# Optimization experiments

Hardware: AMD Instinct MI355X
Metric: run time of the kernel (lower is better)

Reference implementation:

```python
import jax, jax.numpy as jnp
import numpy as np

H_DIM = 1024
N_HEADS = 16
HEAD_D = H_DIM // N_HEADS  # 64


def setup_inputs() -> dict:
    key = jax.random.key(0)
    ks = jax.random.split(key, 10)
    B, T, C = 2, 2048, H_DIM
    init = 1.0 / np.sqrt(C)  # lecun_normal-scale stand-in
    src = jax.random.normal(ks[0], (B, T, C), dtype=jnp.float32)
    mask = jnp.ones((B, T), dtype=jnp.float32)  # unused when causal
    Wq = jax.random.normal(ks[1], (C, H_DIM), dtype=jnp.float32) * init
    Wk = jax.random.normal(ks[2], (C, H_DIM), dtype=jnp.float32) * init
    Wv = jax.random.normal(ks[3], (C, H_DIM), dtype=jnp.float32) * init
    Wo = jax.random.normal(ks[4], (H_DIM, H_DIM), dtype=jnp.float32) * init
    bq = jnp.zeros((H_DIM,), jnp.float32)
    bk = jnp.zeros((H_DIM,), jnp.float32)
    bv = jnp.zeros((H_DIM,), jnp.float32)
    bo = jnp.zeros((H_DIM,), jnp.float32)
    return {"src": src, "mask": mask, "Wq": Wq, "bq": bq, "Wk": Wk, "bk": bk,
            "Wv": Wv, "bv": bv, "Wo": Wo, "bo": bo}


def reference(src, mask, Wq, bq, Wk, bk, Wv, bv, Wo, bo):
    # MaskedCausalAttention forward, deterministic=True (dropout = identity),
    # use_causal_mask=True.
    B, T, C = src.shape
    N, D = N_HEADS, HEAD_D
    # q,k,v: [B, N, T, D]
    q = (src @ Wq + bq).reshape(B, T, N, D).transpose(0, 2, 1, 3)
    k = (src @ Wk + bk).reshape(B, T, N, D).transpose(0, 2, 1, 3)
    v = (src @ Wv + bv).reshape(B, T, N, D).transpose(0, 2, 1, 3)
    # scores: [B, N, T, T]
    scores = jnp.einsum('bntd,bnsd->bnts', q, k) / jnp.sqrt(jnp.float32(D))
    causal = jnp.tril(jnp.ones((T, T), dtype=bool))[None, None]
    scores = jnp.where(causal, scores, -jnp.inf)
    probs = jax.nn.softmax(scores, axis=-1)
    attn = jnp.einsum('bnts,bnsd->bntd', probs, v)  # [B, N, T, D]
    attn = attn.transpose(0, 2, 1, 3).reshape(B, T, N * D)
    return attn @ Wo + bo
```

## Files before the change

kernel.cpp:

```cpp
#include <hip/hip_runtime.h>
#include <hip/hip_bf16.h>

typedef __hip_bfloat16 bf16;
typedef __attribute__((ext_vector_type(8))) short short8;
typedef __attribute__((ext_vector_type(4))) float f32x4;

#define BATCH 2
#define SEQ   2048
#define HDIM  1024
#define NHEAD 16
#define DHEAD 64
#define MROWS (BATCH*SEQ)

#define QSCALE 0.18033688f
#define EXP2F(x) __builtin_amdgcn_exp2f(x)

static __device__ __forceinline__ short f2bs(float x) {
    __hip_bfloat16 h = (__hip_bfloat16)x;
    return *reinterpret_cast<short*>(&h);
}
static __device__ __forceinline__ unsigned int pk2(float a, float b) {
    __hip_bfloat162 h = __float22bfloat162_rn(make_float2(a, b));
    return *reinterpret_cast<unsigned int*>(&h);
}

static __device__ __forceinline__ void gload16(const void* g, void* l) {
    __builtin_amdgcn_global_load_lds(
        (const __attribute__((address_space(1))) unsigned int*)g,
        (__attribute__((address_space(3))) unsigned int*)l, 16, 0, 0);
}

__global__ __launch_bounds__(256) void prep1(const float* __restrict__ src,
        const float* __restrict__ Wq, const float* __restrict__ Wk,
        const float* __restrict__ Wv, const float* __restrict__ Wo,
        short* __restrict__ Sb, short* __restrict__ WT,
        short* __restrict__ WoT)
{
    __shared__ float t[64][65];
    const int bx = blockIdx.x, tid = threadIdx.x;
    if (bx < 4096) {
        int i = bx * 256 + tid;
        float4 v = ((const float4*)src)[i];
        ushort4 o;
        o.x = (unsigned short)f2bs(v.x);
        o.y = (unsigned short)f2bs(v.y);
        o.z = (unsigned short)f2bs(v.z);
        o.w = (unsigned short)f2bs(v.w);
        ((ushort4*)Sb)[i] = o;
        return;
    }
    const int tb = bx - 4096;
    const int wsel = tb >> 8;
    const float* W = (wsel == 0) ? Wq : (wsel == 1) ? Wk : (wsel == 2) ? Wv : Wo;
    short* dst = (wsel < 3) ? WT : WoT;
    const int roff = (wsel < 3) ? wsel * 1024 : 0;
    const int t8 = tb & 255;
    const int n0 = (t8 & 15) * 64, k0 = (t8 >> 4) * 64;
#pragma unroll
    for (int i = 0; i < 16; i++) {
        int idx = tid + i * 256, r = idx >> 6, c = idx & 63;
        t[r][c] = W[(size_t)(k0 + r) * HDIM + n0 + c];
    }
    __syncthreads();
#pragma unroll
    for (int i = 0; i < 16; i++) {
        int idx = tid + i * 256, c = idx >> 6, r = idx & 63;
        dst[(size_t)(roff + n0 + c) * HDIM + k0 + r] = f2bs(t[r][c]);
    }
}

__global__ __launch_bounds__(512, 2) void gemm_qkv(const short* __restrict__ A,
        const short* __restrict__ Bt,
        const float* __restrict__ bq, const float* __restrict__ bk,
        const float* __restrict__ bv,
        short* __restrict__ Qout, short* __restrict__ Kout,
        short* __restrict__ Vtout)
{
    __shared__ short SM[2][28672];
    const int tid = threadIdx.x, lane = tid & 63, w = tid >> 6;
    const int quad = lane >> 4, l15 = lane & 15;
    const int m0 = blockIdx.y * 256, n0 = blockIdx.x * 192;
    const int wr = w >> 1, wc = w & 1;

    static const unsigned char CTAB[8][7] = {
        { 0,  1,  2,  3, 32 + 0,  32 + 1,  32 + 6 },
        { 4,  5,  6,  7, 32 + 2,  32 + 3,  32 + 7 },
        { 8,  9, 10, 11, 32 + 4,  32 + 5,  32 + 8 },
        {12, 13, 14, 15, 32 + 12, 32 + 13, 32 + 9 },
        {16, 17, 18, 19, 32 + 14, 32 + 10, 32 + 11},
        {20, 21, 22, 23, 32 + 15, 32 + 18, 32 + 19},
        {24, 25, 26, 27, 32 + 16, 32 + 20, 32 + 21},
        {28, 29, 30, 31, 32 + 17, 32 + 22, 32 + 23}
    };

    const short* gp[7];
    int lo[7];
#pragma unroll
    for (int i = 0; i < 7; i++) {
        int c = CTAB[w][i];
        if (c < 32) {
            gp[i] = A + (size_t)(m0 + (c >> 1) * 16 + l15) * HDIM
                      + (c & 1) * 32 + quad * 8;
            lo[i] = c * 512;
        } else {
            int v = c - 32;
            gp[i] = Bt + (size_t)(n0 + (v >> 1) * 16 + l15) * HDIM
                       + (v & 1) * 32 + quad * 8;
            lo[i] = 16384 + v * 512;
        }
    }

    f32x4 acc[4][6];
#pragma unroll
    for (int i = 0; i < 4; i++)
#pragma unroll
        for (int j = 0; j < 6; j++) acc[i][j] = (f32x4){0.f, 0.f, 0.f, 0.f};

#pragma unroll
    for (int i = 0; i < 7; i++) { gload16(gp[i], &SM[0][lo[i]]); gp[i] += 64; }

    short8 af[4][2];
    for (int t = 0; t < 16; ++t) {
        const short* Tb = SM[t & 1];
        short* Sn = SM[(t + 1) & 1];

        asm volatile("s_waitcnt vmcnt(1)" ::: "memory");
        __builtin_amdgcn_s_barrier();

#pragma unroll
        for (int mi = 0; mi < 4; mi++)
#pragma unroll
            for (int kh = 0; kh < 2; kh++)
                af[mi][kh] = *(const short8*)
                    &Tb[((wr * 4 + mi) * 2 + kh) * 512 + lane * 8];
        short8 bf01[3][2];
#pragma unroll
        for (int nn = 0; nn < 3; nn++)
#pragma unroll
            for (int kh = 0; kh < 2; kh++)
                bf01[nn][kh] = *(const short8*)
                    &Tb[16384 + ((wc * 6 + nn) * 2 + kh) * 512 + lane * 8];

        if (t < 15) {
#pragma unroll
            for (int i = 0; i < 7; i++) { gload16(gp[i], Sn + lo[i]); gp[i] += 64; }
        }

        __builtin_amdgcn_s_setprio(1);
#pragma unroll
        for (int nn = 0; nn < 3; nn++)
#pragma unroll
            for (int mi = 0; mi < 4; mi++)
#pragma unroll
                for (int kh = 0; kh < 2; kh++)
                    acc[mi][nn] = __builtin_amdgcn_mfma_f32_16x16x32_bf16(
                        af[mi][kh], bf01[nn][kh], acc[mi][nn], 0, 0, 0);
        __builtin_amdgcn_s_setprio(0);

        if (t < 15) asm volatile("s_waitcnt vmcnt(7)" ::: "memory");
        else        asm volatile("s_waitcnt vmcnt(0)" ::: "memory");

        short8 bf23[3][2];
#pragma unroll
        for (int nn = 0; nn < 3; nn++)
#pragma unroll
            for (int kh = 0; kh < 2; kh++)
                bf23[nn][kh] = *(const short8*)
                    &Tb[16384 + ((wc * 6 + 3 + nn) * 2 + kh) * 512 + lane * 8];

        __builtin_amdgcn_s_setprio(1);
#pragma unroll
        for (int nn = 0; nn < 3; nn++)
#pragma unroll
            for (int mi = 0; mi < 4; mi++)
#pragma unroll
                for (int kh = 0; kh < 2; kh++)
                    acc[mi][3 + nn] = __builtin_amdgcn_mfma_f32_16x16x32_bf16(
                        af[mi][kh], bf23[nn][kh], acc[mi][3 + nn], 0, 0, 0);
        __builtin_amdgcn_s_setprio(0);
    }

#pragma unroll
    for (int mi = 0; mi < 4; mi++) {
        int mB = m0 + wr * 64 + mi * 16 + quad * 4;
        int bb = mB >> 11, tt = mB & 2047;
#pragma unroll
        for (int ni = 0; ni < 6; ni++) {
            int n = n0 + wc * 96 + ni * 16 + l15;
            int rg = n >> 10, nl = n & 1023;
            if (rg == 0) {
                float bbv = bq[nl];
#pragma unroll
                for (int r = 0; r < 4; r++)
                    Qout[(size_t)(mB + r) * HDIM + nl] =
                        f2bs((acc[mi][ni][r] + bbv) * QSCALE);
            } else if (rg == 1) {
                float bbv = bk[nl];
#pragma unroll
                for (int r = 0; r < 4; r++)
                    Kout[(size_t)(mB + r) * HDIM + nl] =
                        f2bs(acc[mi][ni][r] + bbv);
            } else {
                float bvv = bv[nl];
                int h = nl >> 6, d = nl & 63;
                size_t base = ((size_t)((bb * NHEAD + h) * DHEAD + d)) * SEQ + tt;
                ushort4 pk;
                pk.x = (unsigned short)f2bs(acc[mi][ni][0] + bvv);
                pk.y = (unsigned short)f2bs(acc[mi][ni][1] + bvv);
                pk.z = (unsigned short)f2bs(acc[mi][ni][2] + bvv);
                pk.w = (unsigned short)f2bs(acc[mi][ni][3] + bvv);
                *(ushort4*)(Vtout + base) = pk;
            }
        }
    }
}

__global__ __launch_bounds__(512) void attn_mfma(const short* __restrict__ Qb,
        const short* __restrict__ Kb, const short* __restrict__ Vt,
        short* __restrict__ Ab,
        float* __restrict__ Opart, float* __restrict__ Psum)
{
    __shared__ short SMEM[25600];
    const int tid = threadIdx.x, lane = tid & 63, w = tid >> 6;
    const int quad = lane >> 4, l15 = lane & 15;
    const int L = blockIdx.x;

    static const signed char S_TAB[24] =
        {15,15, 7,14,14,13,13, 6,12,12,11,11, 5,10,10, 9, 9, 4, 8, 8, 3, 2, 1, 0};
    static const signed char H_TAB[24] =
        { 0, 1,-1, 0, 1, 0, 1,-1, 0, 1, 0, 1,-1, 0, 1, 0, 1,-1, 0, 1,-1,-1,-1,-1};

    const int pair = (L & 7) + 8 * ((L >> 3) & 3);
    const int u = L >> 5;
    const int b = pair >> 4, head = pair & 15;
    const int sblk = S_TAB[u];
    const int half = H_TAB[u];
    const int it0   = (half == 1) ? (sblk + 1) : 0;
    const int itEnd = (half == 0) ? (sblk + 1) : (2 * sblk + 2);
    const int nj = itEnd - it0;

    const short* Kbh = Kb + (size_t)b * SEQ * HDIM + head * DHEAD;
    const short* Vth = Vt + (size_t)(b * NHEAD + head) * DHEAD * SEQ;
    short* Pw = SMEM + 16384 + w * 1152;

    const int s_w = 2 * sblk + (w >> 2);
    const int rho = w * 16 + l15;
    const int qr = sblk * 128 + rho;

    const short* qptr = Qb + (size_t)(b * SEQ + qr) * HDIM + head * DHEAD + quad * 8;
    short8 bq0 = *(const short8*)qptr;
    short8 bq1 = *(const short8*)(qptr + 32);

    const short* gp[2];
    int stp[2], ldo[2];
#pragma unroll
    for (int i = 0; i < 2; i++) {
        int c8 = w * 2 + i;
        if (c8 < 8) {
            int t = c8 >> 1, h = c8 & 1;
            gp[i] = Kbh + (size_t)(t * 16 + l15) * HDIM + h * 32 + quad * 8;
            stp[i] = 64 * HDIM;
        } else {
            int c = c8 - 8, dt = c >> 1, kh = c & 1;
            gp[i] = Vth + (size_t)(dt * 16 + l15) * SEQ + kh * 32 + quad * 8;
            stp[i] = 64;
        }
        ldo[i] = c8 * 512;
        gp[i] += (size_t)it0 * stp[i];
    }

    f32x4 o[4];
#pragma unroll
    for (int dt = 0; dt < 4; dt++) o[dt] = (f32x4){0.f, 0.f, 0.f, 0.f};
    float psum = 0.f;

#pragma unroll
    for (int i = 0; i < 2; i++) { gload16(gp[i], &SMEM[ldo[i]]); gp[i] += stp[i]; }

    for (int j = 0; j < nj; ++j) {
        const int cur = j & 1;
        short* Ks = &SMEM[cur * 8192];
        short* Vs = Ks + 4096;

        if (j + 1 < nj) {
            short* nb = &SMEM[(cur ^ 1) * 8192];
#pragma unroll
            for (int i = 0; i < 2; i++) { gload16(gp[i], nb + ldo[i]); gp[i] += stp[i]; }
            asm volatile("s_waitcnt vmcnt(2)" ::: "memory");
        } else {
            asm volatile("s_waitcnt vmcnt(0)" ::: "memory");
        }
        __builtin_amdgcn_s_barrier();

        const int itg = it0 + j;
        const int s0 = itg * 64;
        f32x4 sv[4];
        __builtin_amdgcn_s_setprio(1);
#pragma unroll
        for (int t = 0; t < 4; t++) {
            sv[t] = (f32x4){0.f, 0.f, 0.f, 0.f};
            short8 k0 = *(const short8*)&Ks[(t * 2) * 512 + lane * 8];
            short8 k1 = *(const short8*)&Ks[(t * 2 + 1) * 512 + lane * 8];
            sv[t] = __builtin_amdgcn_mfma_f32_16x16x32_bf16(k0, bq0, sv[t], 0, 0, 0);
            sv[t] = __builtin_amdgcn_mfma_f32_16x16x32_bf16(k1, bq1, sv[t], 0, 0, 0);
        }
        __builtin_amdgcn_s_setprio(0);

        float p[16];
        if (itg >= s_w) {
#pragma unroll
            for (int t = 0; t < 4; t++)
#pragma unroll
                for (int r = 0; r < 4; r++) {
                    int key = s0 + t * 16 + quad * 4 + r;
                    p[t * 4 + r] = (key <= qr) ? EXP2F(sv[t][r]) : 0.f;
                }
        } else {
#pragma unroll
            for (int t = 0; t < 4; t++)
#pragma unroll
                for (int r = 0; r < 4; r++)
                    p[t * 4 + r] = EXP2F(sv[t][r]);
        }
#pragma unroll
        for (int i = 0; i < 16; i++) psum += p[i];

#pragma unroll
        for (int t = 0; t < 4; t++) {
            uint2 u2;
            u2.x = pk2(p[t * 4],     p[t * 4 + 1]);
            u2.y = pk2(p[t * 4 + 2], p[t * 4 + 3]);
            *(uint2*)&Pw[l15 * 72 + t * 16 + quad * 4] = u2;
        }
        short8 bp0 = *(const short8*)&Pw[l15 * 72 + quad * 8];
        short8 bp1 = *(const short8*)&Pw[l15 * 72 + 32 + quad * 8];

        __builtin_amdgcn_s_setprio(1);
#pragma unroll
        for (int dt = 0; dt < 4; dt++) {
            short8 av0 = *(const short8*)&Vs[(dt * 2) * 512 + lane * 8];
            short8 av1 = *(const short8*)&Vs[(dt * 2 + 1) * 512 + lane * 8];
            o[dt] = __builtin_amdgcn_mfma_f32_16x16x32_bf16(av0, bp0, o[dt], 0, 0, 0);
            o[dt] = __builtin_amdgcn_mfma_f32_16x16x32_bf16(av1, bp1, o[dt], 0, 0, 0);
        }
        __builtin_amdgcn_s_setprio(0);
        __builtin_amdgcn_s_barrier();
    }

    float lrow = psum + __shfl_xor(psum, 16);
    lrow += __shfl_xor(lrow, 32);

    if (half >= 0) {
        const int tile = (pair * 8 + (sblk - 8)) * 2 + half;
        float* Ot = Opart + (size_t)tile * 8192;
#pragma unroll
        for (int dt = 0; dt < 4; dt++)
            *(f32x4*)&Ot[rho * 64 + dt * 16 + quad * 4] = o[dt];
        if (quad == 0) Psum[(pair * 8 + (sblk - 8)) * 256 + half * 128 + rho] = lrow;
        return;
    }

    const float inv = 1.f / lrow;
    const size_t obase = (size_t)(b * SEQ + qr) * HDIM + head * DHEAD;
#pragma unroll
    for (int dt = 0; dt < 4; dt++) {
        uint2 u2;
        u2.x = pk2(o[dt][0] * inv, o[dt][1] * inv);
        u2.y = pk2(o[dt][2] * inv, o[dt][3] * inv);
        *(uint2*)&Ab[obase + dt * 16 + quad * 4] = u2;
    }
}

__global__ __launch_bounds__(256) void combine(const float* __restrict__ Opart,
        const float* __restrict__ Psum, short* __restrict__ Ab)
{
    const int bxx = blockIdx.x;
    const int pair = bxx & 31, si = bxx >> 5;
    const int b = pair >> 4, head = pair & 15;
    const int tid = threadIdx.x;
    const int row = tid >> 1, dq = (tid & 1) * 32;

    const size_t t0 = ((size_t)(pair * 8 + si) * 2) * 8192;
    const float* O0 = Opart + t0;
    const float* O1 = O0 + 8192;
    const int p0 = (pair * 8 + si) * 256;
    const float inv = 1.f / (Psum[p0 + row] + Psum[p0 + 128 + row]);

    const int qrow = (8 + si) * 128 + row;
    const size_t obase = (size_t)(b * SEQ + qrow) * HDIM + head * DHEAD + dq;
#pragma unroll
    for (int g = 0; g < 8; g++) {
        float4 a = *(const float4*)&O0[row * 64 + dq + g * 4];
        float4 c = *(const float4*)&O1[row * 64 + dq + g * 4];
        ushort4 pk;
        pk.x = (unsigned short)f2bs((a.x + c.x) * inv);
        pk.y = (unsigned short)f2bs((a.y + c.y) * inv);
        pk.z = (unsigned short)f2bs((a.z + c.z) * inv);
        pk.w = (unsigned short)f2bs((a.w + c.w) * inv);
        *(ushort4*)&Ab[obase + g * 4] = pk;
    }
}

__global__ __launch_bounds__(512) void gemm_o(const short* __restrict__ A,
        const short* __restrict__ Bt, const float* __restrict__ bo,
        float* __restrict__ Out)
{
    __shared__ short SM[2 * 16384];
    const int tid = threadIdx.x, lane = tid & 63, w = tid >> 6;
    const int quad = lane >> 4, l15 = lane & 15;
    const int m0 = blockIdx.y * 128, n0 = blockIdx.x * 128;
    const int wr = w >> 2, wc = w & 3;

    const short* gsrc[4];
    short* ldst[4];
#pragma unroll
    for (int i = 0; i < 4; i++) {
        int c8 = w * 4 + i;
        if (c8 < 16) {
            gsrc[i] = A + (size_t)(m0 + (c8 >> 1) * 16 + l15) * HDIM
                        + (c8 & 1) * 32 + quad * 8;
            ldst[i] = &SM[c8 * 512];
        } else {
            int v = c8 - 16;
            gsrc[i] = Bt + (size_t)(n0 + (v >> 1) * 16 + l15) * HDIM
                         + (v & 1) * 32 + quad * 8;
            ldst[i] = &SM[8192 + v * 512];
        }
    }

    f32x4 acc[4][2];
#pragma unroll
    for (int i = 0; i < 4; i++)
#pragma unroll
        for (int j = 0; j < 2; j++) acc[i][j] = (f32x4){0.f, 0.f, 0.f, 0.f};

#pragma unroll
    for (int i = 0; i < 4; i++) { gload16(gsrc[i], ldst[i]); gsrc[i] += 64; }

    for (int kk = 0; kk < 16; ++kk) {
        const int cur = kk & 1;
        if (kk < 15) {
            const int nb = (cur ^ 1) * 16384;
#pragma unroll
            for (int i = 0; i < 4; i++) { gload16(gsrc[i], ldst[i] + nb); gsrc[i] += 64; }
            asm volatile("s_waitcnt vmcnt(4)" ::: "memory");
        } else {
            asm volatile("s_waitcnt vmcnt(0)" ::: "memory");
        }
        __builtin_amdgcn_s_barrier();

        const short* Asb = &SM[cur * 16384];
        const short* Bsb = Asb + 8192;
#pragma unroll
        for (int kh = 0; kh < 2; kh++) {
            short8 af[4], bfr[2];
#pragma unroll
            for (int mi = 0; mi < 4; mi++)
                af[mi] = *(const short8*)&Asb[((wr * 4 + mi) * 2 + kh) * 512 + lane * 8];
#pragma unroll
            for (int ni = 0; ni < 2; ni++)
                bfr[ni] = *(const short8*)&Bsb[((wc * 2 + ni) * 2 + kh) * 512 + lane * 8];
#pragma unroll
            for (int mi = 0; mi < 4; mi++)
#pragma unroll
                for (int ni = 0; ni < 2; ni++)
                    acc[mi][ni] = __builtin_amdgcn_mfma_f32_16x16x32_bf16(
                                      af[mi], bfr[ni], acc[mi][ni], 0, 0, 0);
        }
        __builtin_amdgcn_s_barrier();
    }

#pragma unroll
    for (int mi = 0; mi < 4; mi++) {
        int mB = m0 + (wr * 4 + mi) * 16 + quad * 4;
#pragma unroll
        for (int ni = 0; ni < 2; ni++) {
            int n = n0 + (wc * 2 + ni) * 16 + l15;
            float bb = bo[n];
#pragma unroll
            for (int r = 0; r < 4; r++)
                Out[(size_t)(mB + r) * HDIM + n] = acc[mi][ni][r] + bb;
        }
    }
}

extern "C" void kernel_launch(void* const* d_in, const int* in_sizes, int n_in,
                              void* d_out, int out_size, void* d_ws, size_t ws_size,
                              hipStream_t stream)
{
    const float* src = (const float*)d_in[0];
    const float* Wq = (const float*)d_in[2];
    const float* bq = (const float*)d_in[3];
    const float* Wk = (const float*)d_in[4];
    const float* bk = (const float*)d_in[5];
    const float* Wv = (const float*)d_in[6];
    const float* bv = (const float*)d_in[7];
    const float* Wo = (const float*)d_in[8];
    const float* bo = (const float*)d_in[9];
    float* out = (float*)d_out;

    short* Sb   = (short*)d_ws;
    short* Qb   = Sb + (size_t)MROWS * HDIM;
    short* Kb   = Qb + (size_t)MROWS * HDIM;
    short* Vt   = Kb + (size_t)MROWS * HDIM;
    short* WoT  = Vt + (size_t)MROWS * HDIM;
    short* WT   = (short*)d_out;
    short* Ab   = Qb;
    float* Opart = (float*)d_out;
    float* Psum  = (float*)Sb;

    prep1<<<dim3(4096 + 1024), dim3(256), 0, stream>>>(src, Wq, Wk, Wv, Wo, Sb, WT, WoT);

    gemm_qkv<<<dim3(16, 16), dim3(512), 0, stream>>>(Sb, WT, bq, bk, bv, Qb, Kb, Vt);

    attn_mfma<<<dim3(768), dim3(512), 0, stream>>>(Qb, Kb, Vt, Ab, Opart, Psum);

    combine<<<dim3(256), dim3(256), 0, stream>>>(Opart, Psum, Ab);

    gemm_o<<<dim3(8, 32), dim3(512), 0, stream>>>(Ab, WoT, bo, out);
}
```

Before: 192.6 us.

## Double attention query tile to 256 rows with 1024-thread blocks

Each attention block now covers 256 query rows with 16 waves instead of 128 rows with 8 waves. This halves the grid and lets each K/V tile loaded into shared memory be reused by twice as many query rows, with one load per wave per iteration. The schedule tables, split-half ranges, partial-output layout and combine kernel are rescaled to match. In exchange there are fewer blocks to balance across CUs, the work per block is coarser, and the larger LDS footprint and 1024-thread blocks may lower occupancy.

```diff
diff --git a/kernel.cpp b/kernel.cpp
--- a/kernel.cpp
+++ b/kernel.cpp
@@ -215,58 +215,55 @@
     }
 }
 
-__global__ __launch_bounds__(512) void attn_mfma(const short* __restrict__ Qb,
+__global__ __launch_bounds__(1024) void attn_mfma(const short* __restrict__ Qb,
         const short* __restrict__ Kb, const short* __restrict__ Vt,
         short* __restrict__ Ab,
         float* __restrict__ Opart, float* __restrict__ Psum)
 {
-    __shared__ short SMEM[25600];
+    __shared__ short SMEM[34816];
     const int tid = threadIdx.x, lane = tid & 63, w = tid >> 6;
     const int quad = lane >> 4, l15 = lane & 15;
     const int L = blockIdx.x;
 
-    static const signed char S_TAB[24] =
-        {15,15, 7,14,14,13,13, 6,12,12,11,11, 5,10,10, 9, 9, 4, 8, 8, 3, 2, 1, 0};
-    static const signed char H_TAB[24] =
-        { 0, 1,-1, 0, 1, 0, 1,-1, 0, 1, 0, 1,-1, 0, 1, 0, 1,-1, 0, 1,-1,-1,-1,-1};
+    static const signed char S_TAB[12] = {7,7,3,6,6,5,5,2,4,4,1,0};
+    static const signed char H_TAB[12] = {0,1,-1,0,1,0,1,-1,0,1,-1,-1};
 
     const int pair = (L & 7) + 8 * ((L >> 3) & 3);
     const int u = L >> 5;
     const int b = pair >> 4, head = pair & 15;
     const int sblk = S_TAB[u];
     const int half = H_TAB[u];
-    const int it0   = (half == 1) ? (sblk + 1) : 0;
-    const int itEnd = (half == 0) ? (sblk + 1) : (2 * sblk + 2);
+    const int it0   = (half == 1) ? (2 * sblk + 2) : 0;
+    const int itEnd = (half == 0) ? (2 * sblk + 2) : (4 * sblk + 4);
     const int nj = itEnd - it0;
 
     const short* Kbh = Kb + (size_t)b * SEQ * HDIM + head * DHEAD;
     const short* Vth = Vt + (size_t)(b * NHEAD + head) * DHEAD * SEQ;
     short* Pw = SMEM + 16384 + w * 1152;
 
-    const int s_w = 2 * sblk + (w >> 2);
+    const int s_w = 4 * sblk + (w >> 2);
     const int rho = w * 16 + l15;
-    const int qr = sblk * 128 + rho;
+    const int qr = sblk * 256 + rho;
 
     const short* qptr = Qb + (size_t)(b * SEQ + qr) * HDIM + head * DHEAD + quad * 8;
     short8 bq0 = *(const short8*)qptr;
     short8 bq1 = *(const short8*)(qptr + 32);
 
-    const short* gp[2];
-    int stp[2], ldo[2];
-#pragma unroll
-    for (int i = 0; i < 2; i++) {
-        int c8 = w * 2 + i;
+    const short* gp0;
+    int stp0, ldo0;
+    {
+        int c8 = w;
         if (c8 < 8) {
             int t = c8 >> 1, h = c8 & 1;
-            gp[i] = Kbh + (size_t)(t * 16 + l15) * HDIM + h * 32 + quad * 8;
-            stp[i] = 64 * HDIM;
+            gp0 = Kbh + (size_t)(t * 16 + l15) * HDIM + h * 32 + quad * 8;
+            stp0 = 64 * HDIM;
         } else {
             int c = c8 - 8, dt = c >> 1, kh = c & 1;
-            gp[i] = Vth + (size_t)(dt * 16 + l15) * SEQ + kh * 32 + quad * 8;
-            stp[i] = 64;
-        }
-        ldo[i] = c8 * 512;
-        gp[i] += (size_t)it0 * stp[i];
+            gp0 = Vth + (size_t)(dt * 16 + l15) * SEQ + kh * 32 + quad * 8;
+            stp0 = 64;
+        }
+        ldo0 = c8 * 512;
+        gp0 += (size_t)it0 * stp0;
     }
 
     f32x4 o[4];
@@ -274,8 +271,7 @@
     for (int dt = 0; dt < 4; dt++) o[dt] = (f32x4){0.f, 0.f, 0.f, 0.f};
     float psum = 0.f;
 
-#pragma unroll
-    for (int i = 0; i < 2; i++) { gload16(gp[i], &SMEM[ldo[i]]); gp[i] += stp[i]; }
+    gload16(gp0, &SMEM[ldo0]); gp0 += stp0;
 
     for (int j = 0; j < nj; ++j) {
         const int cur = j & 1;
@@ -283,10 +279,8 @@
         short* Vs = Ks + 4096;
 
         if (j + 1 < nj) {
-            short* nb = &SMEM[(cur ^ 1) * 8192];
-#pragma unroll
-            for (int i = 0; i < 2; i++) { gload16(gp[i], nb + ldo[i]); gp[i] += stp[i]; }
-            asm volatile("s_waitcnt vmcnt(2)" ::: "memory");
+            gload16(gp0, &SMEM[(cur ^ 1) * 8192 + ldo0]); gp0 += stp0;
+            asm volatile("s_waitcnt vmcnt(1)" ::: "memory");
         } else {
             asm volatile("s_waitcnt vmcnt(0)" ::: "memory");
         }
@@ -351,12 +345,12 @@
     lrow += __shfl_xor(lrow, 32);
 
     if (half >= 0) {
-        const int tile = (pair * 8 + (sblk - 8)) * 2 + half;
-        float* Ot = Opart + (size_t)tile * 8192;
+        const int strip = pair * 4 + (sblk - 4);
+        float* Ot = Opart + ((size_t)(strip * 2 + half)) * 16384;
 #pragma unroll
         for (int dt = 0; dt < 4; dt++)
             *(f32x4*)&Ot[rho * 64 + dt * 16 + quad * 4] = o[dt];
-        if (quad == 0) Psum[(pair * 8 + (sblk - 8)) * 256 + half * 128 + rho] = lrow;
+        if (quad == 0) Psum[strip * 512 + half * 256 + rho] = lrow;
         return;
     }
 
@@ -377,21 +371,19 @@
     const int bxx = blockIdx.x;
     const int pair = bxx & 31, si = bxx >> 5;
     const int b = pair >> 4, head = pair & 15;
-    const int tid = threadIdx.x;
-    const int row = tid >> 1, dq = (tid & 1) * 32;
-
-    const size_t t0 = ((size_t)(pair * 8 + si) * 2) * 8192;
-    const float* O0 = Opart + t0;
-    const float* O1 = O0 + 8192;
-    const int p0 = (pair * 8 + si) * 256;
-    const float inv = 1.f / (Psum[p0 + row] + Psum[p0 + 128 + row]);
-
-    const int qrow = (8 + si) * 128 + row;
-    const size_t obase = (size_t)(b * SEQ + qrow) * HDIM + head * DHEAD + dq;
-#pragma unroll
-    for (int g = 0; g < 8; g++) {
-        float4 a = *(const float4*)&O0[row * 64 + dq + g * 4];
-        float4 c = *(const float4*)&O1[row * 64 + dq + g * 4];
+    const int row = threadIdx.x;
+
+    const int strip = pair * 4 + si;
+    const float* O0 = Opart + ((size_t)(strip * 2)) * 16384;
+    const float* O1 = O0 + 16384;
+    const float inv = 1.f / (Psum[strip * 512 + row] + Psum[strip * 512 + 256 + row]);
+
+    const int qrow = (4 + si) * 256 + row;
+    const size_t obase = (size_t)(b * SEQ + qrow) * HDIM + head * DHEAD;
+#pragma unroll
+    for (int g = 0; g < 16; g++) {
+        float4 a = *(const float4*)&O0[row * 64 + g * 4];
+        float4 c = *(const float4*)&O1[row * 64 + g * 4];
         ushort4 pk;
         pk.x = (unsigned short)f2bs((a.x + c.x) * inv);
         pk.y = (unsigned short)f2bs((a.y + c.y) * inv);
@@ -513,9 +505,9 @@
 
     gemm_qkv<<<dim3(16, 16), dim3(512), 0, stream>>>(Sb, WT, bq, bk, bv, Qb, Kb, Vt);
 
-    attn_mfma<<<dim3(768), dim3(512), 0, stream>>>(Qb, Kb, Vt, Ab, Opart, Psum);
-
-    combine<<<dim3(256), dim3(256), 0, stream>>>(Opart, Psum, Ab);
+    attn_mfma<<<dim3(384), dim3(1024), 0, stream>>>(Qb, Kb, Vt, Ab, Opart, Psum);
+
+    combine<<<dim3(128), dim3(256), 0, stream>>>(Opart, Psum, Ab);
 
     gemm_o<<<dim3(8, 32), dim3(512), 0, stream>>>(Ab, WoT, bo, out);
 }
```

After: 203.1 us. +5.5%, slower.
